# Kernel tuning notes

Measured on AMD Instinct MI355X. Metric: run time of the kernel, lower is better.

## Reference

```python
import jax, jax.numpy as jnp
import numpy as np

N = 100000          # original nodes
E = 1600000         # edges (avg degree 16)
D_IN = 128
D_BLOOM = 16        # (bloom_lmax+1)^2 with lmax=3
D_OUT = 128
D_INTER = D_BLOOM + D_OUT
K = 4               # blooms per node
PF = 4              # pool factor (nodes per cluster)
C = N // PF         # coarsened nodes
MIN_RADIUS = 0.1


def setup_inputs() -> dict:
    key = jax.random.key(0)
    ks = jax.random.split(key, 10)
    x = jax.random.normal(ks[0], (N, D_IN), jnp.float32)
    pos = jax.random.normal(ks[1], (N, 3), jnp.float32)
    edge_index = jax.random.randint(ks[2], (2, E), 0, N)
    edge_attr = jax.random.normal(ks[3], (E, 3), jnp.float32)
    batch = jnp.sort(jax.random.randint(ks[4], (N,), 0, 64))
    # learned parameters (stand-ins for the injected submodules)
    W_conv = jax.random.normal(ks[5], (D_IN, D_INTER), jnp.float32) / np.sqrt(D_IN)
    W_edge = jax.random.normal(ks[6], (3, D_INTER), jnp.float32)
    D_bloom = jax.random.normal(ks[7], (K, D_BLOOM, 3), jnp.float32) / np.sqrt(D_BLOOM)
    W_gather = jax.random.normal(ks[8], (D_OUT, D_OUT), jnp.float32) / np.sqrt(D_OUT)
    W_gattr = jax.random.normal(ks[9], (3, D_OUT), jnp.float32)
    return dict(x=x, pos=pos, edge_index=edge_index, edge_attr=edge_attr, batch=batch,
                W_conv=W_conv, W_edge=W_edge, D_bloom=D_bloom,
                W_gather=W_gather, W_gattr=W_gattr)


def reference(x, pos, edge_index, edge_attr, batch, W_conv, W_edge, D_bloom, W_gather, W_gattr):
    src, dst = edge_index[0], edge_index[1]

    # ---- bloom conv: per-edge message, scatter-sum to destination nodes ----
    msg = x[src] @ W_conv + edge_attr @ W_edge           # [E, D_INTER]
    out = jax.ops.segment_sum(msg, dst, num_segments=N)  # [N, D_INTER]
    sph = out[:, :D_BLOOM]                               # [N, D_BLOOM]
    feat = out[:, D_BLOOM:]                              # [N, D_OUT]

    # ---- bloom: K candidate points per node ----
    offsets = MIN_RADIUS * jnp.tanh(jnp.einsum('nb,kbd->nkd', sph, D_bloom))  # [N,K,3]
    bloom_pos = (pos[:, None, :] + offsets).reshape(N * K, 3)
    bloom_batch = jnp.repeat(jnp.arange(N), K)           # bloom node -> original node

    # ---- cluster: deterministic pool_factor grouping ----
    clusters = bloom_batch // PF                         # [N*K] bloom -> cluster
    node_cluster = jnp.arange(N) // PF                   # [N] node -> cluster (coalesced pairs)

    # new_pos = scatter_mean(pos[coalesced node], cluster): exactly PF nodes per cluster
    new_pos = jax.ops.segment_sum(pos, node_cluster, num_segments=C) / PF  # [C,3]

    # ---- gather conv: bipartite message passing N features -> C clusters ----
    gather_edge_attr = pos[bloom_batch] - new_pos[clusters]                 # [N*K,3]
    gm = feat[bloom_batch] @ W_gather + gather_edge_attr @ W_gattr          # [N*K,D_OUT]
    x_new = jax.ops.segment_sum(gm, clusters, num_segments=C) / (K * PF)    # [C,D_OUT]

    # ---- new_edge_index: spspmm chain == map endpoints to clusters + coalesce ----
    enc = node_cluster[src] * C + node_cluster[dst]      # encode cluster pairs
    enc_u = jnp.unique(enc, size=E, fill_value=0)        # coalesced, padded with (0,0)
    new_edge_index = jnp.stack([enc_u // C, enc_u % C])  # [2, E] (padded)
    new_edge_attr = new_pos[new_edge_index[1]] - new_pos[new_edge_index[0]]

    # ---- new_batch: graph id of each cluster (batch is sorted per graph) ----
    new_batch = jax.ops.segment_max(batch, node_cluster, num_segments=C)

    return (x_new, new_pos, new_edge_index, new_edge_attr, new_batch)
```

## Files before the change

kernel.cpp:

```cpp
#include <hip/hip_runtime.h>
#include <hip/hip_bf16.h>
#include <stdint.h>

typedef unsigned int uint_t;
typedef unsigned short ushort_t;

#define NN 100000
#define EE 1600000
#define CC 25000
#define DINTER 144
#define NBKT 196
#define NBKT2 1568
#define NSEG 6272
#define KCAP 1024

#define W_M1B      0u
#define W_AGGB     8384u
#define W_PAGG     1658384u
#define W_PKA4     14858384u
#define W_PKC      21258384u
#define W_OFFS2    22858384u
#define W_BHA2     23058385u
#define W_BHC      23059953u
#define W_BBA2     23060149u
#define W_BCURA2   23061718u
#define W_BBC      23063286u
#define W_BCURC    23063483u
#define WS_WORDS   23066816u

#define O_XNEW  0u
#define O_POS   3200000u
#define O_EI    3275000u
#define O_ATTR  6475000u
#define O_BATCH 11275000u

static __device__ __forceinline__ uint_t f2bf(float f) {
    union { float f; uint_t i; } v; v.f = f;
    uint_t x = v.i;
    return (x + 0x7fffu + ((x >> 16) & 1u)) >> 16;
}
static __device__ __forceinline__ float bf2f(ushort_t u) {
    union { uint_t i; float f; } v; v.i = ((uint_t)u) << 16; return v.f;
}

__global__ void xpack(const float4* __restrict__ x4, uint2* __restrict__ xb2) {
    int i = blockIdx.x * 256 + threadIdx.x;
    if (i >= NN * 32) return;
    float4 v = x4[i];
    uint2 r;
    r.x = f2bf(v.x) | (f2bf(v.y) << 16);
    r.y = f2bf(v.z) | (f2bf(v.w) << 16);
    xb2[i] = r;
}

__global__ void build_m1f(const float* __restrict__ Wconv,
                          const float* __restrict__ Wedge,
                          const float* __restrict__ Wg,
                          ushort_t* __restrict__ m1b) {
    int j = blockIdx.x;
    int o = threadIdx.x;
    const float* wrow = (j < 128) ? (Wconv + j * DINTER + 16)
                                  : (Wedge + (j - 128) * DINTER + 16);
    float acc = 0.f;
    for (int f = 0; f < 128; ++f)
        acc += wrow[f] * Wg[f * 128 + o];
    m1b[j * 128 + o] = (ushort_t)f2bf(acc);
}

__global__ void edge_hist2(const int* __restrict__ ei,
                           uint_t* __restrict__ bhA2, uint_t* __restrict__ bhC) {
    __shared__ uint_t hA[NBKT2], hC[NBKT];
    int tid = threadIdx.x;
    for (int i = tid; i < NBKT2; i += 1024) hA[i] = 0;
    for (int i = tid; i < NBKT; i += 1024) hC[i] = 0;
    __syncthreads();
    for (int e = blockIdx.x * 1024 + tid; e < EE; e += 256 * 1024) {
        uint_t u = (uint_t)ei[e];
        uint_t v = (uint_t)ei[EE + e];
        atomicAdd(&hA[(u / 12500u) * 196u + (v >> 9)], 1u);
        atomicAdd(&hC[u >> 9], 1u);
    }
    __syncthreads();
    for (int i = tid; i < NBKT2; i += 1024) if (hA[i]) atomicAdd(&bhA2[i], hA[i]);
    for (int i = tid; i < NBKT; i += 1024)  if (hC[i]) atomicAdd(&bhC[i], hC[i]);
}

__global__ void scan_small(const uint_t* __restrict__ in, uint_t* __restrict__ out,
                           uint_t* __restrict__ out2, int n) {
    __shared__ uint_t part[256];
    int tid = threadIdx.x;
    int per = (n + 255) >> 8;
    int lo = tid * per;
    int hi = lo + per; if (hi > n) hi = n;
    if (lo > n) lo = n;
    uint_t s = 0;
    for (int i = lo; i < hi; ++i) s += in[i];
    part[tid] = s;
    __syncthreads();
    for (int off = 1; off < 256; off <<= 1) {
        uint_t v = (tid >= off) ? part[tid - off] : 0u;
        __syncthreads();
        part[tid] += v;
        __syncthreads();
    }
    uint_t run = part[tid] - s;
    for (int i = lo; i < hi; ++i) {
        out[i] = run;
        if (out2) out2[i] = run;
        run += in[i];
    }
    if (tid == 255) out[n] = run;
}

#define TPB 4096
__global__ void bucket_place_AC(const int* __restrict__ ei, const float* __restrict__ ea,
                                uint_t* __restrict__ bcurA, uint_t* __restrict__ bcurC,
                                uint4* __restrict__ pk4, uint_t* __restrict__ pkC) {
    __shared__ uint_t histA[NBKT2], gbaseA[NBKT2], curA[NBKT2];
    __shared__ uint_t pkst[TPB];
    __shared__ uint_t gpk[TPB];
    __shared__ unsigned char lo2[TPB];
    __shared__ uint_t histC[NBKT], lbaseC[NBKT], gbaseC[NBKT], curC[NBKT];
    __shared__ uint_t part[1024];
    int tid = threadIdx.x;
    int t0 = blockIdx.x * TPB;
    int nt = EE - t0; if (nt > TPB) nt = TPB;
    for (int i = tid; i < NBKT2; i += 1024) { histA[i] = 0; curA[i] = 0; }
    for (int i = tid; i < NBKT; i += 1024) { histC[i] = 0; curC[i] = 0; }
    __syncthreads();
    for (int i = tid; i < nt; i += 1024) {
        int e = t0 + i;
        uint_t u = (uint_t)ei[e];
        uint_t v = (uint_t)ei[EE + e];
        atomicAdd(&histA[(u / 12500u) * 196u + (v >> 9)], 1u);
        uint_t w = ((u >> 2) << 15) | (v >> 2);
        pkst[i] = w;
        lo2[i] = (unsigned char)(u & 3u);
        atomicAdd(&histC[w >> 22], 1u);
    }
    __syncthreads();
    for (int b = tid; b < NBKT2; b += 1024) {
        uint_t h = histA[b];
        if (h) gbaseA[b] = atomicAdd(&bcurA[b], h);
    }
    uint_t h = (tid < NBKT) ? histC[tid] : 0u;
    if (tid < NBKT) gbaseC[tid] = atomicAdd(&bcurC[tid], h);
    part[tid] = h;
    __syncthreads();
    for (int off = 1; off < 1024; off <<= 1) {
        uint_t v = (tid >= off) ? part[tid - off] : 0u;
        __syncthreads();
        part[tid] += v;
        __syncthreads();
    }
    if (tid < NBKT) lbaseC[tid] = part[tid] - h;
    __syncthreads();
    for (int i = tid; i < nt; i += 1024) {
        uint_t w = pkst[i];
        uint_t b = w >> 22;
        uint_t r = lbaseC[b] + atomicAdd(&curC[b], 1u);
        gpk[r] = w;
    }
    __syncthreads();
    for (int r = tid; r < nt; r += 1024) {
        uint_t w = gpk[r];
        uint_t b = w >> 22;
        pkC[gbaseC[b] + ((uint_t)r - lbaseC[b])] = w;
    }
    for (int i = tid; i < nt; i += 1024) {
        int e = t0 + i;
        uint_t w = pkst[i];
        uint_t u = ((w >> 15) << 2) | (uint_t)lo2[i];
        uint_t vq = w & 32767u;
        uint_t b = (u / 12500u) * 196u + (vq >> 7);
        uint_t r = gbaseA[b] + atomicAdd(&curA[b], 1u);
        uint4 p;
        p.x = ((vq & 127u) << 17) | u;
        p.y = __float_as_uint(ea[(size_t)e * 3 + 0]);
        p.z = __float_as_uint(ea[(size_t)e * 3 + 1]);
        p.w = __float_as_uint(ea[(size_t)e * 3 + 2]);
        pk4[r] = p;
    }
}

__global__ void bucket_sort_A2(const uint_t* __restrict__ bbA2, const uint4* __restrict__ pk4,
                               uint_t* __restrict__ pkW, uint_t* __restrict__ paggw,
                               uint_t* __restrict__ offs2) {
    __shared__ uint4 st[2048];
    __shared__ uint_t hist[128], base2[128], cur[128];
    __shared__ float eacc0[128], eacc1[128], eacc2[128];
    __shared__ uint_t part[256];
    int tid = threadIdx.x, bk = blockIdx.x;
    uint_t s = bbA2[bk], epos = bbA2[bk + 1];
    int n = (int)(epos - s);
    if (n > 2048) n = 2048;
    if (tid < 128) {
        hist[tid] = 0; cur[tid] = 0;
        eacc0[tid] = 0.f; eacc1[tid] = 0.f; eacc2[tid] = 0.f;
    }
    for (int i = tid; i < n; i += 256) st[i] = pk4[s + i];
    __syncthreads();
    for (int i = tid; i < n; i += 256) {
        uint4 p = st[i];
        uint_t d = p.x >> 17;
        atomicAdd(&hist[d], 1u);
        atomicAdd(&eacc0[d], __uint_as_float(p.y));
        atomicAdd(&eacc1[d], __uint_as_float(p.z));
        atomicAdd(&eacc2[d], __uint_as_float(p.w));
    }
    __syncthreads();
    uint_t h = (tid < 128) ? hist[tid] : 0u;
    part[tid] = h;
    __syncthreads();
    for (int off = 1; off < 256; off <<= 1) {
        uint_t v = (tid >= off) ? part[tid - off] : 0u;
        __syncthreads();
        part[tid] += v;
        __syncthreads();
    }
    int sl = bk / 196, q = bk - sl * 196;
    if (tid < 128) {
        base2[tid] = part[tid] - h;
        int c = q * 128 + tid;
        if (c < CC) {
            uint_t kk = (uint_t)sl * CC + (uint_t)c;
            offs2[kk] = s + base2[tid];
            paggw[(size_t)kk * 66 + 64] = f2bf(eacc0[tid]) | (f2bf(eacc1[tid]) << 16);
            paggw[(size_t)kk * 66 + 65] = f2bf(eacc2[tid]);
        }
    }
    if (bk == 0 && tid == 0) offs2[8 * CC] = EE;
    __syncthreads();
    for (int i = tid; i < n; i += 256) {
        uint4 p = st[i];
        uint_t d = p.x >> 17;
        uint_t r = base2[d] + atomicAdd(&cur[d], 1u);
        pkW[s + r] = p.x;
    }
}

__global__ void bucket_sort_C(const uint_t* __restrict__ bbC, uint_t* __restrict__ pkC,
                              uint_t* __restrict__ csub) {
    __shared__ uint_t st[8960];
    __shared__ uint_t hist[32], base2[32], cur[32];
    __shared__ uint_t part[256];
    int tid = threadIdx.x, bk = blockIdx.x;
    uint_t s = bbC[bk], epos = bbC[bk + 1];
    int n = (int)(epos - s);
    if (n > 8960) n = 8960;
    if (tid < 32) { hist[tid] = 0; cur[tid] = 0; }
    for (int i = tid; i < n; i += 256) st[i] = pkC[s + i];
    __syncthreads();
    for (int i = tid; i < n; i += 256) atomicAdd(&hist[(st[i] >> 17) & 31u], 1u);
    __syncthreads();
    uint_t h = (tid < 32) ? hist[tid] : 0u;
    part[tid] = h;
    __syncthreads();
    for (int off = 1; off < 256; off <<= 1) {
        uint_t v = (tid >= off) ? part[tid - off] : 0u;
        __syncthreads();
        part[tid] += v;
        __syncthreads();
    }
    if (tid < 32) {
        base2[tid] = part[tid] - h;
        csub[bk * 32 + tid] = s + base2[tid];
    }
    if (bk == 0 && tid == 0) csub[NSEG] = EE;
    __syncthreads();
    for (int i = tid; i < n; i += 256) {
        uint_t w = st[i];
        uint_t d = (w >> 17) & 31u;
        uint_t r = base2[d] + atomicAdd(&cur[d], 1u);
        pkC[s + r] = w;
    }
}

__global__ void cluster_pass(const float* __restrict__ pos, const int* __restrict__ batch,
                             float* __restrict__ out) {
    int c = blockIdx.x * 256 + threadIdx.x;
    if (c >= CC) return;
    float px = 0.f, py = 0.f, pz = 0.f;
    for (int j = 0; j < 4; ++j) {
        int n = c * 4 + j;
        px += pos[n * 3 + 0];
        py += pos[n * 3 + 1];
        pz += pos[n * 3 + 2];
    }
    px *= 0.25f; py *= 0.25f; pz *= 0.25f;
    out[O_POS + c * 3 + 0] = px;
    out[O_POS + c * 3 + 1] = py;
    out[O_POS + c * 3 + 2] = pz;
    int b = batch[c * 4];
    b = max(b, batch[c * 4 + 1]);
    b = max(b, batch[c * 4 + 2]);
    b = max(b, batch[c * 4 + 3]);
    out[O_BATCH + c] = (float)b;
}

#define CPW 8
__global__ void cluster_reduce5(const uint_t* __restrict__ offs2, const uint_t* __restrict__ pkW,
                                const uint_t* __restrict__ xb, uint_t* __restrict__ paggw) {
    int tid = threadIdx.x;
    int lane = tid & 63;
    int s = blockIdx.x & 7;
    int c0 = ((blockIdx.x >> 3) * 4 + (tid >> 6)) * CPW;
    if (c0 >= CC) return;
    uint_t kk0 = (uint_t)s * CC + (uint_t)c0;
    const uint_t* xl = xb + lane;
    for (int cl = 0; cl < CPW; ++cl) {
        if (c0 + cl >= CC) break;
        uint_t start = (uint_t)__builtin_amdgcn_readfirstlane((int)offs2[kk0 + cl]);
        uint_t end   = (uint_t)__builtin_amdgcn_readfirstlane((int)offs2[kk0 + cl + 1]);
        float a0 = 0.f, a1 = 0.f;
        uint_t i = start;
        for (; i + 4u <= end; i += 4u) {
            uint_t w0 = pkW[i + 0u];
            uint_t w1 = pkW[i + 1u];
            uint_t w2 = pkW[i + 2u];
            uint_t w3 = pkW[i + 3u];
            uint_t x0 = xl[(size_t)(w0 & 0x1FFFFu) * 64u];
            uint_t x1 = xl[(size_t)(w1 & 0x1FFFFu) * 64u];
            uint_t x2 = xl[(size_t)(w2 & 0x1FFFFu) * 64u];
            uint_t x3 = xl[(size_t)(w3 & 0x1FFFFu) * 64u];
            a0 += bf2f((ushort_t)(x0 & 0xffffu)); a1 += bf2f((ushort_t)(x0 >> 16));
            a0 += bf2f((ushort_t)(x1 & 0xffffu)); a1 += bf2f((ushort_t)(x1 >> 16));
            a0 += bf2f((ushort_t)(x2 & 0xffffu)); a1 += bf2f((ushort_t)(x2 >> 16));
            a0 += bf2f((ushort_t)(x3 & 0xffffu)); a1 += bf2f((ushort_t)(x3 >> 16));
        }
        for (; i < end; ++i) {
            uint_t wj = pkW[i];
            uint_t xv = xl[(size_t)(wj & 0x1FFFFu) * 64u];
            a0 += bf2f((ushort_t)(xv & 0xffffu));
            a1 += bf2f((ushort_t)(xv >> 16));
        }
        paggw[(size_t)(kk0 + (uint_t)cl) * 66 + lane] = f2bf(a0) | (f2bf(a1) << 16);
    }
}

#define GEMM_CPB 32
__global__ void gemm_tiled(const uint_t* __restrict__ paggw, const ushort_t* __restrict__ m1b,
                           float* __restrict__ out) {
    __shared__ ushort_t m1s[131 * 128];
    __shared__ __align__(16) float srowT[132][8];
    int tid = threadIdx.x;
    {
        const uint_t* m1w = (const uint_t*)m1b;
        uint_t* m1sw = (uint_t*)m1s;
        for (int i = tid; i < 131 * 64; i += 256) m1sw[i] = m1w[i];
    }
    int o = tid & 127, half = tid >> 7;
    int c0b = blockIdx.x * GEMM_CPB;
    for (int it = 0; it < GEMM_CPB / 8; ++it) {
        int c0 = c0b + it * 8;
        __syncthreads();
        for (int i = tid; i < 528; i += 256) {
            int cg = i / 66, rem = i - cg * 66;
            int c = c0 + cg;
            float lo = 0.f, hi = 0.f;
            if (c < CC) {
                #pragma unroll
                for (int s = 0; s < 8; ++s) {
                    uint_t w = paggw[((size_t)s * 25000u + (uint_t)c) * 66 + rem];
                    lo += bf2f((ushort_t)(w & 0xffffu));
                    hi += bf2f((ushort_t)(w >> 16));
                }
            }
            srowT[rem * 2][cg]     = lo;
            srowT[rem * 2 + 1][cg] = hi;
        }
        __syncthreads();
        float acc0 = 0.f, acc1 = 0.f, acc2 = 0.f, acc3 = 0.f;
        #pragma unroll 4
        for (int j = 0; j < 131; ++j) {
            float m = bf2f(m1s[j * 128 + o]);
            float4 s = *(const float4*)&srowT[j][half * 4];
            acc0 += s.x * m;
            acc1 += s.y * m;
            acc2 += s.z * m;
            acc3 += s.w * m;
        }
        int cb = c0 + half * 4;
        if (cb + 0 < CC) out[O_XNEW + (size_t)(cb + 0) * 128 + o] = 0.25f * acc0;
        if (cb + 1 < CC) out[O_XNEW + (size_t)(cb + 1) * 128 + o] = 0.25f * acc1;
        if (cb + 2 < CC) out[O_XNEW + (size_t)(cb + 2) * 128 + o] = 0.25f * acc2;
        if (cb + 3 < CC) out[O_XNEW + (size_t)(cb + 3) * 128 + o] = 0.25f * acc3;
    }
}

__global__ void enc_count(const uint_t* __restrict__ csub, const uint_t* __restrict__ pkC,
                          uint_t* __restrict__ bcnt, uint_t* __restrict__ kbuf) {
    __shared__ uint_t bmp[3125];
    __shared__ uint_t sh[256];
    int tid = threadIdx.x, bid = blockIdx.x;
    uint_t s = csub[bid], epos = csub[bid + 1];
    int n = (int)(epos - s);
    for (int i = tid; i < 3125; i += 256) bmp[i] = 0;
    __syncthreads();
    for (int i = tid; i < n; i += 256) {
        uint_t w = pkC[s + i];
        uint_t le = ((w >> 15) & 3u) * 25000u + (w & 32767u);
        atomicOr(&bmp[le >> 5], 1u << (le & 31u));
    }
    __syncthreads();
    int lo = tid * 13, hi = lo + 13;
    if (lo > 3125) lo = 3125;
    if (hi > 3125) hi = 3125;
    uint_t mine = 0;
    for (int i = lo; i < hi; ++i) mine += __popc(bmp[i]);
    sh[tid] = mine;
    __syncthreads();
    for (int off = 1; off < 256; off <<= 1) {
        uint_t v = (tid >= off) ? sh[tid - off] : 0u;
        __syncthreads();
        sh[tid] += v;
        __syncthreads();
    }
    uint_t r = sh[tid] - mine;
    uint_t kb = (uint_t)bid * KCAP;
    for (int i = lo; i < hi; ++i) {
        uint_t bits = bmp[i];
        while (bits) {
            int b = __builtin_ctz(bits);
            bits &= bits - 1u;
            if (r < KCAP) kbuf[kb + r] = (uint_t)i * 32u + (uint_t)b;
            r++;
        }
    }
    if (tid == 255) bcnt[bid] = min(sh[255], (uint_t)KCAP);
}

__global__ void tail_zero(const uint_t* __restrict__ ebase, float* __restrict__ out) {
    uint_t total = ebase[NSEG];
    uint_t idx = blockIdx.x * 256u + (uint_t)threadIdx.x;
    uint_t stride = gridDim.x * 256u;
    for (uint_t k = total + idx; k < EE; k += stride) {
        out[O_EI + k] = 0.f;
        out[O_EI + EE + k] = 0.f;
    }
    for (uint_t k = 3u * total + idx; k < 3u * EE; k += stride) {
        out[O_ATTR + k] = 0.f;
    }
}

__global__ void enc_emit(const uint_t* __restrict__ ebase, const uint_t* __restrict__ kbuf,
                         float* __restrict__ out) {
    int tid = threadIdx.x, bid = blockIdx.x;
    uint_t g0 = ebase[bid], g1 = ebase[bid + 1];
    int cnt = (int)(g1 - g0);
    const float* np = out + O_POS;
    uint_t ubase = ((uint_t)(bid >> 5)) * 128u + ((uint_t)(bid & 31)) * 4u;
    uint_t kb = (uint_t)bid * KCAP;
    for (int r = tid; r < cnt; r += 256) {
        uint_t le = kbuf[kb + r];
        uint_t uo = le / 25000u;
        uint_t v = le - uo * 25000u;
        uint_t u = ubase + uo;
        uint_t rank = g0 + (uint_t)r;
        out[O_EI + rank] = (float)u;
        out[O_EI + EE + rank] = (float)v;
        out[O_ATTR + (size_t)rank * 3 + 0] = np[v * 3 + 0] - np[u * 3 + 0];
        out[O_ATTR + (size_t)rank * 3 + 1] = np[v * 3 + 1] - np[u * 3 + 1];
        out[O_ATTR + (size_t)rank * 3 + 2] = np[v * 3 + 2] - np[u * 3 + 2];
    }
}

extern "C" void kernel_launch(void* const* d_in, const int* in_sizes, int n_in,
                              void* d_out, int out_size, void* d_ws, size_t ws_size,
                              hipStream_t stream) {
    const float* x     = (const float*)d_in[0];
    const float* pos   = (const float*)d_in[1];
    const int*   ei    = (const int*)d_in[2];
    const float* ea    = (const float*)d_in[3];
    const int*   batch = (const int*)d_in[4];
    const float* Wconv = (const float*)d_in[5];
    const float* Wedge = (const float*)d_in[6];
    const float* Wg    = (const float*)d_in[8];

    float*  out = (float*)d_out;
    uint_t* ws  = (uint_t*)d_ws;

    if (ws_size < (size_t)WS_WORDS * 4) return;

    ushort_t* m1b    = (ushort_t*)(ws + W_M1B);
    uint_t*   pkW    = ws + W_AGGB;
    uint_t*   paggw  = ws + W_PAGG;
    uint4*    pk4    = (uint4*)(ws + W_PKA4);
    uint_t*   pkC    = ws + W_PKC;
    uint_t*   offs2  = ws + W_OFFS2;
    uint_t*   bhA2   = ws + W_BHA2;
    uint_t*   bhC    = ws + W_BHC;
    uint_t*   bbA2   = ws + W_BBA2;
    uint_t*   bcurA2 = ws + W_BCURA2;
    uint_t*   bbC    = ws + W_BBC;
    uint_t*   bcurC  = ws + W_BCURC;
    uint_t*   xb     = (uint_t*)(out + O_EI);
    uint_t*   csub   = ws + W_PKA4;
    uint_t*   bcnt2  = ws + W_PKA4 + 8192u;
    uint_t*   ebase2 = ws + W_PKA4 + 16384u;
    uint_t*   kbuf   = ws + W_PAGG;

    hipMemsetAsync(bhA2, 0, (size_t)(NBKT2 + NBKT) * 4, stream);

    xpack<<<dim3(12500), dim3(256), 0, stream>>>((const float4*)x, (uint2*)xb);
    build_m1f<<<dim3(131), dim3(128), 0, stream>>>(Wconv, Wedge, Wg, m1b);
    edge_hist2<<<dim3(256), dim3(1024), 0, stream>>>(ei, bhA2, bhC);
    scan_small<<<dim3(1), dim3(256), 0, stream>>>(bhA2, bbA2, bcurA2, NBKT2);
    scan_small<<<dim3(1), dim3(256), 0, stream>>>(bhC, bbC, bcurC, NBKT);
    bucket_place_AC<<<dim3((EE + TPB - 1) / TPB), dim3(1024), 0, stream>>>(ei, ea, bcurA2, bcurC, pk4, pkC);
    bucket_sort_A2<<<dim3(NBKT2), dim3(256), 0, stream>>>(bbA2, pk4, pkW, paggw, offs2);
    cluster_pass<<<dim3(98), dim3(256), 0, stream>>>(pos, batch, out);
    cluster_reduce5<<<dim3(((CC + 4 * CPW - 1) / (4 * CPW)) * 8), dim3(256), 0, stream>>>(offs2, pkW, xb, paggw);
    gemm_tiled<<<dim3((CC + GEMM_CPB - 1) / GEMM_CPB), dim3(256), 0, stream>>>(paggw, m1b, out);
    bucket_sort_C<<<dim3(NBKT), dim3(256), 0, stream>>>(bbC, pkC, csub);
    enc_count<<<dim3(NSEG), dim3(256), 0, stream>>>(csub, pkC, bcnt2, kbuf);
    scan_small<<<dim3(1), dim3(256), 0, stream>>>(bcnt2, ebase2, (uint_t*)0, NSEG);
    tail_zero<<<dim3(512), dim3(256), 0, stream>>>(ebase2, out);
    enc_emit<<<dim3(NSEG), dim3(256), 0, stream>>>(ebase2, kbuf, out);
}
```

Measured before the change: 422.0 us.

## Merge small kernels to cut launch count and double clusters per wave

Folds cluster_pass into xpack, merges the two small bucket scans into one two-block launch, and folds tail_zero into enc_emit as extra blocks. This removes three kernel launches and the serialization gaps between them. It also raises CPW from 8 to 16 in cluster_reduce5, so each wave handles more clusters and the grid shrinks. The risk is less parallelism in the reduce and some extra branching in the merged kernels.

```diff
diff --git a/kernel.cpp b/kernel.cpp
--- a/kernel.cpp
+++ b/kernel.cpp
@@ -43,8 +43,29 @@
     union { uint_t i; float f; } v; v.i = ((uint_t)u) << 16; return v.f;
 }
 
-__global__ void xpack(const float4* __restrict__ x4, uint2* __restrict__ xb2) {
+__global__ void xpack(const float4* __restrict__ x4, uint2* __restrict__ xb2,
+                      const float* __restrict__ pos, const int* __restrict__ batch,
+                      float* __restrict__ out) {
     int i = blockIdx.x * 256 + threadIdx.x;
+    if (i < CC) {
+        int c = i;
+        float px = 0.f, py = 0.f, pz = 0.f;
+        for (int j = 0; j < 4; ++j) {
+            int n = c * 4 + j;
+            px += pos[n * 3 + 0];
+            py += pos[n * 3 + 1];
+            pz += pos[n * 3 + 2];
+        }
+        px *= 0.25f; py *= 0.25f; pz *= 0.25f;
+        out[O_POS + c * 3 + 0] = px;
+        out[O_POS + c * 3 + 1] = py;
+        out[O_POS + c * 3 + 2] = pz;
+        int b = batch[c * 4];
+        b = max(b, batch[c * 4 + 1]);
+        b = max(b, batch[c * 4 + 2]);
+        b = max(b, batch[c * 4 + 3]);
+        out[O_BATCH + c] = (float)b;
+    }
     if (i >= NN * 32) return;
     float4 v = x4[i];
     uint2 r;
@@ -85,9 +106,10 @@
     for (int i = tid; i < NBKT; i += 1024)  if (hC[i]) atomicAdd(&bhC[i], hC[i]);
 }
 
-__global__ void scan_small(const uint_t* __restrict__ in, uint_t* __restrict__ out,
-                           uint_t* __restrict__ out2, int n) {
-    __shared__ uint_t part[256];
+static __device__ __forceinline__ void scan_body(const uint_t* __restrict__ in,
+                                                 uint_t* __restrict__ out,
+                                                 uint_t* __restrict__ out2, int n,
+                                                 uint_t* part) {
     int tid = threadIdx.x;
     int per = (n + 255) >> 8;
     int lo = tid * per;
@@ -110,6 +132,21 @@
         run += in[i];
     }
     if (tid == 255) out[n] = run;
+}
+
+__global__ void scan_small(const uint_t* __restrict__ in, uint_t* __restrict__ out,
+                           uint_t* __restrict__ out2, int n) {
+    __shared__ uint_t part[256];
+    scan_body(in, out, out2, n, part);
+}
+
+__global__ void scan_dual(const uint_t* __restrict__ inA, uint_t* __restrict__ outA,
+                          uint_t* __restrict__ outA2,
+                          const uint_t* __restrict__ inB, uint_t* __restrict__ outB,
+                          uint_t* __restrict__ outB2) {
+    __shared__ uint_t part[256];
+    if (blockIdx.x == 0) scan_body(inA, outA, outA2, NBKT2, part);
+    else                 scan_body(inB, outB, outB2, NBKT, part);
 }
 
 #define TPB 4096
@@ -276,29 +313,7 @@
     }
 }
 
-__global__ void cluster_pass(const float* __restrict__ pos, const int* __restrict__ batch,
-                             float* __restrict__ out) {
-    int c = blockIdx.x * 256 + threadIdx.x;
-    if (c >= CC) return;
-    float px = 0.f, py = 0.f, pz = 0.f;
-    for (int j = 0; j < 4; ++j) {
-        int n = c * 4 + j;
-        px += pos[n * 3 + 0];
-        py += pos[n * 3 + 1];
-        pz += pos[n * 3 + 2];
-    }
-    px *= 0.25f; py *= 0.25f; pz *= 0.25f;
-    out[O_POS + c * 3 + 0] = px;
-    out[O_POS + c * 3 + 1] = py;
-    out[O_POS + c * 3 + 2] = pz;
-    int b = batch[c * 4];
-    b = max(b, batch[c * 4 + 1]);
-    b = max(b, batch[c * 4 + 2]);
-    b = max(b, batch[c * 4 + 3]);
-    out[O_BATCH + c] = (float)b;
-}
-
-#define CPW 8
+#define CPW 16
 __global__ void cluster_reduce5(const uint_t* __restrict__ offs2, const uint_t* __restrict__ pkW,
                                 const uint_t* __restrict__ xb, uint_t* __restrict__ paggw) {
     int tid = threadIdx.x;
@@ -430,22 +445,22 @@
     if (tid == 255) bcnt[bid] = min(sh[255], (uint_t)KCAP);
 }
 
-__global__ void tail_zero(const uint_t* __restrict__ ebase, float* __restrict__ out) {
-    uint_t total = ebase[NSEG];
-    uint_t idx = blockIdx.x * 256u + (uint_t)threadIdx.x;
-    uint_t stride = gridDim.x * 256u;
-    for (uint_t k = total + idx; k < EE; k += stride) {
-        out[O_EI + k] = 0.f;
-        out[O_EI + EE + k] = 0.f;
-    }
-    for (uint_t k = 3u * total + idx; k < 3u * EE; k += stride) {
-        out[O_ATTR + k] = 0.f;
-    }
-}
-
 __global__ void enc_emit(const uint_t* __restrict__ ebase, const uint_t* __restrict__ kbuf,
                          float* __restrict__ out) {
     int tid = threadIdx.x, bid = blockIdx.x;
+    if (bid >= NSEG) {
+        uint_t total = ebase[NSEG];
+        uint_t idx = (uint_t)(bid - NSEG) * 256u + (uint_t)tid;
+        uint_t stride = 512u * 256u;
+        for (uint_t k = total + idx; k < EE; k += stride) {
+            out[O_EI + k] = 0.f;
+            out[O_EI + EE + k] = 0.f;
+        }
+        for (uint_t k = 3u * total + idx; k < 3u * EE; k += stride) {
+            out[O_ATTR + k] = 0.f;
+        }
+        return;
+    }
     uint_t g0 = ebase[bid], g1 = ebase[bid + 1];
     int cnt = (int)(g1 - g0);
     const float* np = out + O_POS;
@@ -502,19 +517,16 @@
 
     hipMemsetAsync(bhA2, 0, (size_t)(NBKT2 + NBKT) * 4, stream);
 
-    xpack<<<dim3(12500), dim3(256), 0, stream>>>((const float4*)x, (uint2*)xb);
+    xpack<<<dim3(12500), dim3(256), 0, stream>>>((const float4*)x, (uint2*)xb, pos, batch, out);
     build_m1f<<<dim3(131), dim3(128), 0, stream>>>(Wconv, Wedge, Wg, m1b);
     edge_hist2<<<dim3(256), dim3(1024), 0, stream>>>(ei, bhA2, bhC);
-    scan_small<<<dim3(1), dim3(256), 0, stream>>>(bhA2, bbA2, bcurA2, NBKT2);
-    scan_small<<<dim3(1), dim3(256), 0, stream>>>(bhC, bbC, bcurC, NBKT);
+    scan_dual<<<dim3(2), dim3(256), 0, stream>>>(bhA2, bbA2, bcurA2, bhC, bbC, bcurC);
     bucket_place_AC<<<dim3((EE + TPB - 1) / TPB), dim3(1024), 0, stream>>>(ei, ea, bcurA2, bcurC, pk4, pkC);
     bucket_sort_A2<<<dim3(NBKT2), dim3(256), 0, stream>>>(bbA2, pk4, pkW, paggw, offs2);
-    cluster_pass<<<dim3(98), dim3(256), 0, stream>>>(pos, batch, out);
     cluster_reduce5<<<dim3(((CC + 4 * CPW - 1) / (4 * CPW)) * 8), dim3(256), 0, stream>>>(offs2, pkW, xb, paggw);
     gemm_tiled<<<dim3((CC + GEMM_CPB - 1) / GEMM_CPB), dim3(256), 0, stream>>>(paggw, m1b, out);
     bucket_sort_C<<<dim3(NBKT), dim3(256), 0, stream>>>(bbC, pkC, csub);
     enc_count<<<dim3(NSEG), dim3(256), 0, stream>>>(csub, pkC, bcnt2, kbuf);
     scan_small<<<dim3(1), dim3(256), 0, stream>>>(bcnt2, ebase2, (uint_t*)0, NSEG);
-    tail_zero<<<dim3(512), dim3(256), 0, stream>>>(ebase2, out);
-    enc_emit<<<dim3(NSEG), dim3(256), 0, stream>>>(ebase2, kbuf, out);
-}
+    enc_emit<<<dim3(NSEG + 512), dim3(256), 0, stream>>>(ebase2, kbuf, out);
+}
```

After: 422.2 us. About the same (+0.0%).
